# Kernel tuning notes

Measured on AMD Instinct MI355X. Metric: run time of the kernel, lower is better.

The kernel has to match this reference:

```python
import jax, jax.numpy as jnp
import numpy as np

TEMPERATURE = 0.07
N, D, NUM_CLASSES = 8192, 1024, 128


def setup_inputs() -> dict:
    key = jax.random.key(0)
    k1, k2 = jax.random.split(key)
    embeddings = jax.random.normal(k1, (N, D), dtype=jnp.float32)
    labels = jax.random.randint(k2, (N,), 0, NUM_CLASSES, dtype=jnp.int64)
    return {"embeddings": embeddings, "labels": labels}


def reference(embeddings, labels):
    # L2-normalize rows (eps matches F.normalize default clamp of 1e-12 on the norm)
    norm = jnp.maximum(jnp.linalg.norm(embeddings, axis=-1, keepdims=True), 1e-12)
    emb = embeddings / norm
    # [N, N] similarity scaled by temperature
    sim = jnp.matmul(emb, emb.T) / TEMPERATURE
    # positive mask: same label, diagonal zeroed
    pos_mask = (labels[:, None] == labels[None, :]).astype(sim.dtype)
    pos_mask = pos_mask * (1.0 - jnp.eye(sim.shape[0], dtype=sim.dtype))
    exp_sim = jnp.exp(sim)
    sum_exp = exp_sim.sum(axis=1)              # [N]
    pos_sum = (exp_sim * pos_mask).sum(axis=1)  # [N]
    loss = -jnp.log(pos_sum / sum_exp)
    return loss.mean()
```

## Files before the change

kernel.cpp:

```cpp
#include <hip/hip_runtime.h>
#include <hip/hip_bf16.h>
#include <math.h>

#define N 8192
#define D 1024
#define BM 256
#define BK 64
#define NQUART 64
#define NFULL 512
#define NBLK (NQUART + NFULL)
#define ITERS 8

typedef __bf16 bf16_t;
typedef bf16_t bf16x4 __attribute__((ext_vector_type(4)));
typedef bf16_t bf16x8 __attribute__((ext_vector_type(8)));
typedef float f32x4 __attribute__((ext_vector_type(4)));

__global__ __launch_bounds__(256) void norm_cast(const float* __restrict__ in,
                                                 bf16_t* __restrict__ out,
                                                 float* __restrict__ sumExp,
                                                 float* __restrict__ posSum) {
    const int wave = threadIdx.x >> 6, lane = threadIdx.x & 63;
    const int row  = blockIdx.x * 4 + wave;
    const float4* src = (const float4*)(in + (size_t)row * D);
    float4 v[4];
    float ss = 0.f;
    #pragma unroll
    for (int i = 0; i < 4; ++i) {
        v[i] = src[lane + 64 * i];
        ss += v[i].x * v[i].x + v[i].y * v[i].y + v[i].z * v[i].z + v[i].w * v[i].w;
    }
    #pragma unroll
    for (int off = 32; off >= 1; off >>= 1) ss += __shfl_xor(ss, off, 64);
    const float scale = 1.0f / fmaxf(sqrtf(ss), 1e-12f);
    bf16x4* dst = (bf16x4*)(out + (size_t)row * D);
    #pragma unroll
    for (int i = 0; i < 4; ++i) {
        bf16x4 o;
        o[0] = (bf16_t)(v[i].x * scale);
        o[1] = (bf16_t)(v[i].y * scale);
        o[2] = (bf16_t)(v[i].z * scale);
        o[3] = (bf16_t)(v[i].w * scale);
        dst[lane + 64 * i] = o;
    }
    if (lane == 0) { sumExp[row] = 0.f; posSum[row] = 0.f; }
}

__global__ __launch_bounds__(512, 2) void gemm_fused(const bf16_t* __restrict__ E,
                                                     const int* __restrict__ labels,
                                                     float* __restrict__ sumExp,
                                                     float* __restrict__ posSum) {
    __shared__ bf16_t As[2][2][128 * 64];
    __shared__ bf16_t Bs[2][2][128 * 64];

    const int tid  = threadIdx.x;
    const int wave = tid >> 6;
    const int lane = tid & 63;
    const int lr   = lane & 15;
    const int q    = lane >> 4;
    const float invT = 1.0f / 0.07f;

    const int su0 = ((0 + q) ^ (lane & 7)) * 16;
    const int su1 = ((4 + q) ^ (lane & 7)) * 16;

    #define PHASE_MID() do {                                                             \
        __builtin_amdgcn_s_barrier();                                                    \
        asm volatile("s_waitcnt lgkmcnt(0)");                                            \
        __builtin_amdgcn_sched_barrier(0);                                               \
        __builtin_amdgcn_s_setprio(1);                                                   \
    } while (0)
    #define PHASE_END() do {                                                             \
        __builtin_amdgcn_s_setprio(0);                                                   \
        __builtin_amdgcn_s_barrier();                                                    \
    } while (0)

    if (blockIdx.x < NQUART) {
        const int qb = ((int)blockIdx.x & 7) * 8 + ((int)blockIdx.x >> 3);
        const int p  = qb >> 2, qd = qb & 3;
        const int rowStart = 31 * BM + (qd >> 1) * 128;
        const int colStart = p * BM + (qd & 1) * 128;
        const int wm2 = wave >> 2;
        const int wn2 = wave & 3;

        f32x4 acc[4][2];
        #pragma unroll
        for (int m = 0; m < 4; ++m) { acc[m][0] = {0,0,0,0}; acc[m][1] = {0,0,0,0}; }

        const int r0  = tid >> 3;
        const int lu0 = (tid & 7) ^ (r0 & 7);
        const char* gA = (const char*)(E + (size_t)rowStart * D) + (size_t)r0 * (D * 2) + lu0 * 16;
        const char* gB = (const char*)(E + (size_t)colStart * D) + (size_t)r0 * (D * 2) + lu0 * 16;

        #define QSTAGE(buf, kb) do {                                                     \
            const char* ga_ = gA + (kb);                                                 \
            const char* gb_ = gB + (kb);                                                 \
            char* la_ = (char*)&As[buf][0][0] + wave * 1024;                             \
            char* lb_ = (char*)&Bs[buf][0][0] + wave * 1024;                             \
            __builtin_amdgcn_global_load_lds((const __attribute__((address_space(1))) void*)ga_, \
                (__attribute__((address_space(3))) void*)la_, 16, 0, 0);                 \
            __builtin_amdgcn_global_load_lds(                                            \
                (const __attribute__((address_space(1))) void*)(ga_ + 64 * 2048),        \
                (__attribute__((address_space(3))) void*)(la_ + 8192), 16, 0, 0);        \
            __builtin_amdgcn_global_load_lds((const __attribute__((address_space(1))) void*)gb_, \
                (__attribute__((address_space(3))) void*)lb_, 16, 0, 0);                 \
            __builtin_amdgcn_global_load_lds(                                            \
                (const __attribute__((address_space(1))) void*)(gb_ + 64 * 2048),        \
                (__attribute__((address_space(3))) void*)(lb_ + 8192), 16, 0, 0);        \
        } while (0)

        bf16x8 qa[4], qbf[2];
        #define QLD(SU, BUF) do {                                                        \
            const char* aB_ = (const char*)&As[BUF][0][0] + (wm2 * 64 + lr) * 128 + (SU);\
            const char* bB_ = (const char*)&Bs[BUF][0][0] + (wn2 * 32 + lr) * 128 + (SU);\
            _Pragma("unroll")                                                            \
            for (int m_ = 0; m_ < 4; ++m_)                                               \
                qa[m_] = *(const bf16x8*)(aB_ + m_ * 2048);                              \
            qbf[0] = *(const bf16x8*)(bB_);                                              \
            qbf[1] = *(const bf16x8*)(bB_ + 2048);                                       \
        } while (0)
        #define QMFMA() do {                                                             \
            _Pragma("unroll")                                                            \
            for (int m_ = 0; m_ < 4; ++m_) {                                             \
                _Pragma("unroll")                                                        \
                for (int n_ = 0; n_ < 2; ++n_)                                           \
                    acc[m_][n_] = __builtin_amdgcn_mfma_f32_16x16x32_bf16(               \
                        qa[m_], qbf[n_], acc[m_][n_], 0, 0, 0);                          \
            }                                                                            \
        } while (0)

        QSTAGE(0, 0);
        asm volatile("s_waitcnt vmcnt(0)" ::: "memory");
        __builtin_amdgcn_sched_barrier(0);
        __builtin_amdgcn_s_barrier();

        #pragma unroll 1
        for (int it = 0; it < 16; ++it) {
            const int buf = it & 1;
            QLD(su0, buf);
            if (it < 15) QSTAGE(buf ^ 1, (it + 1) * 128);
            PHASE_MID();
            QMFMA();
            PHASE_END();
            QLD(su1, buf);
            asm volatile("s_waitcnt vmcnt(0)" ::: "memory");
            __builtin_amdgcn_sched_barrier(0);
            PHASE_MID();
            QMFMA();
            PHASE_END();
        }

        int lc[2];
        lc[0] = labels[colStart + wn2 * 32 + lr];
        lc[1] = labels[colStart + wn2 * 32 + 16 + lr];
        float colAll[2] = {0.f, 0.f}, colPos[2] = {0.f, 0.f};
        #pragma unroll
        for (int m = 0; m < 4; ++m) {
            #pragma unroll
            for (int e = 0; e < 4; ++e) {
                const int gi = rowStart + wm2 * 64 + m * 16 + q * 4 + e;
                const int li = labels[gi];
                float s_all = 0.f, s_pos = 0.f;
                #pragma unroll
                for (int n = 0; n < 2; ++n) {
                    const float v = __expf(acc[m][n][e] * invT);
                    const bool same = (lc[n] == li);
                    s_all += v;
                    if (same) s_pos += v;
                    colAll[n] += v;
                    if (same) colPos[n] += v;
                }
                #pragma unroll
                for (int off = 1; off < 16; off <<= 1) {
                    s_all += __shfl_xor(s_all, off, 64);
                    s_pos += __shfl_xor(s_pos, off, 64);
                }
                if (lr == 0) {
                    atomicAdd(&sumExp[gi], s_all);
                    atomicAdd(&posSum[gi], s_pos);
                }
            }
        }
        #pragma unroll
        for (int n = 0; n < 2; ++n) {
            float a = colAll[n], pp = colPos[n];
            a += __shfl_xor(a, 16, 64);  a += __shfl_xor(a, 32, 64);
            pp += __shfl_xor(pp, 16, 64); pp += __shfl_xor(pp, 32, 64);
            if (q == 0) {
                const int gj = colStart + wn2 * 32 + n * 16 + lr;
                atomicAdd(&sumExp[gj], a);
                atomicAdd(&posSum[gj], pp);
            }
        }
        return;
    }

    const int f0 = (int)blockIdx.x - NQUART;
    const int f  = (f0 & 7) * (NFULL / 8) + (f0 >> 3);
    const int b  = (f < 496) ? f : f + 16;

    int ti = (int)((sqrtf(8.0f * (float)b + 1.0f) - 1.0f) * 0.5f);
    while ((ti + 1) * (ti + 2) / 2 <= b) ++ti;
    while (ti * (ti + 1) / 2 > b) --ti;
    const int tj = b - ti * (ti + 1) / 2;
    const bool isDiag = (ti == tj);

    const int wm   = wave >> 2;
    const int wn   = wave & 3;
    const int rowStart = ti * BM;
    const int colStart = tj * BM;

    f32x4 acc[8][4];
    #pragma unroll
    for (int m = 0; m < 8; ++m)
        #pragma unroll
        for (int n = 0; n < 4; ++n) acc[m][n] = {0.f, 0.f, 0.f, 0.f};

    const int r0  = tid >> 3;
    const int lu0 = (tid & 7) ^ (r0 & 7);
    const char* gA = (const char*)(E + (size_t)rowStart * D) + (size_t)r0 * (D * 2) + lu0 * 16;
    const char* gB = (const char*)(E + (size_t)colStart * D) + (size_t)r0 * (D * 2) + lu0 * 16;

    #define STAGE_A(buf, h, kb) do {                                                     \
        const char* g0_ = gA + (size_t)(h) * (128 * 2048) + (kb);                        \
        char* l0_ = (char*)&As[buf][h][0] + wave * 1024;                                 \
        __builtin_amdgcn_global_load_lds((const __attribute__((address_space(1))) void*)g0_, \
            (__attribute__((address_space(3))) void*)l0_, 16, 0, 0);                     \
        __builtin_amdgcn_global_load_lds(                                                \
            (const __attribute__((address_space(1))) void*)(g0_ + 64 * 2048),            \
            (__attribute__((address_space(3))) void*)(l0_ + 8192), 16, 0, 0);            \
    } while (0)
    #define STAGE_B(buf, h, kb) do {                                                     \
        const char* g0_ = gB + (size_t)(h) * (128 * 2048) + (kb);                        \
        char* l0_ = (char*)&Bs[buf][h][0] + wave * 1024;                                 \
        __builtin_amdgcn_global_load_lds((const __attribute__((address_space(1))) void*)g0_, \
            (__attribute__((address_space(3))) void*)l0_, 16, 0, 0);                     \
        __builtin_amdgcn_global_load_lds(                                                \
            (const __attribute__((address_space(1))) void*)(g0_ + 64 * 2048),            \
            (__attribute__((address_space(3))) void*)(l0_ + 8192), 16, 0, 0);            \
    } while (0)

    const char* rA0 = (const char*)&As[0][wm][0] + lr * 128;
    const char* rA1 = (const char*)&As[1][wm][0] + lr * 128;
    const char* rB0 = (const char*)&Bs[0][wn >> 1][0] + (wn & 1) * 8192 + lr * 128;
    const char* rB1 = (const char*)&Bs[1][wn >> 1][0] + (wn & 1) * 8192 + lr * 128;

    #define LD_A4(DST, RBASE, MOFFB, SU) do {                                            \
        _Pragma("unroll")                                                                \
        for (int m_ = 0; m_ < 4; ++m_)                                                   \
            DST[m_] = *(const bf16x8*)((RBASE) + (MOFFB) + m_ * 2048 + (SU));            \
    } while (0)
    #define LD_B4(DST, RBASE, SU) do {                                                   \
        _Pragma("unroll")                                                                \
        for (int n_ = 0; n_ < 4; ++n_)                                                   \
            DST[n_] = *(const bf16x8*)((RBASE) + n_ * 2048 + (SU));                      \
    } while (0)
    #define MFMA_QUAD(AF, BF, MO) do {                                                   \
        _Pragma("unroll")                                                                \
        for (int m_ = 0; m_ < 4; ++m_) {                                                 \
            _Pragma("unroll")                                                            \
            for (int n_ = 0; n_ < 4; ++n_)                                               \
                acc[(MO) + m_][n_] = __builtin_amdgcn_mfma_f32_16x16x32_bf16(            \
                    AF[m_], BF[n_], acc[(MO) + m_][n_], 0, 0, 0);                        \
        }                                                                                \
    } while (0)

    bf16x8 a0[4], a1[4], bq0[4], bq1[4];

    STAGE_B(0, 0, 0);  STAGE_B(0, 1, 0);
    STAGE_A(0, 0, 0);  STAGE_A(0, 1, 0);
    STAGE_B(1, 0, 128); STAGE_B(1, 1, 128);
    asm volatile("s_waitcnt vmcnt(4)" ::: "memory");
    __builtin_amdgcn_sched_barrier(0);
    __builtin_amdgcn_s_barrier();

    #pragma unroll 1
    for (int it = 0; it < ITERS; ++it) {
        const bool lastIt = (it == ITERS - 1);
        const int kb1 = (2 * it + 1) * 128;
        const int kb2 = (2 * it + 2) * 128;
        const int kb3 = (2 * it + 3) * 128;

        LD_A4(a0, rA0, 0, su0);
        LD_B4(bq0, rB0, su0);
        STAGE_A(1, 0, kb1);
        PHASE_MID();
        MFMA_QUAD(a0, bq0, 0);
        PHASE_END();

        LD_A4(a1, rA0, 0, su1);
        LD_B4(bq1, rB0, su1);
        STAGE_A(1, 1, kb1);
        PHASE_MID();
        MFMA_QUAD(a1, bq1, 0);
        PHASE_END();

        LD_A4(a0, rA0, 8192, su0);
        if (!lastIt) STAGE_B(0, 0, kb2);
        PHASE_MID();
        MFMA_QUAD(a0, bq0, 4);
        PHASE_END();

        LD_A4(a1, rA0, 8192, su1);
        if (!lastIt) {
            STAGE_B(0, 1, kb2);
            asm volatile("s_waitcnt vmcnt(4)" ::: "memory");
        } else {
            asm volatile("s_waitcnt vmcnt(0)" ::: "memory");
        }
        __builtin_amdgcn_sched_barrier(0);
        PHASE_MID();
        MFMA_QUAD(a1, bq1, 4);
        PHASE_END();

        LD_A4(a0, rA1, 0, su0);
        LD_B4(bq0, rB1, su0);
        if (!lastIt) STAGE_A(0, 0, kb2);
        PHASE_MID();
        MFMA_QUAD(a0, bq0, 0);
        PHASE_END();

        LD_A4(a1, rA1, 0, su1);
        LD_B4(bq1, rB1, su1);
        if (!lastIt) STAGE_A(0, 1, kb2);
        PHASE_MID();
        MFMA_QUAD(a1, bq1, 0);
        PHASE_END();

        LD_A4(a0, rA1, 8192, su0);
        if (!lastIt) STAGE_B(1, 0, kb3);
        PHASE_MID();
        MFMA_QUAD(a0, bq0, 4);
        PHASE_END();

        LD_A4(a1, rA1, 8192, su1);
        if (!lastIt) {
            STAGE_B(1, 1, kb3);
            asm volatile("s_waitcnt vmcnt(4)" ::: "memory");
            __builtin_amdgcn_sched_barrier(0);
        }
        PHASE_MID();
        MFMA_QUAD(a1, bq1, 4);
        PHASE_END();
    }

    int lc[4];
    #pragma unroll
    for (int n = 0; n < 4; ++n)
        lc[n] = labels[colStart + wn * 64 + n * 16 + lr];

    float colAll[4] = {0.f, 0.f, 0.f, 0.f};
    float colPos[4] = {0.f, 0.f, 0.f, 0.f};
    #pragma unroll
    for (int m = 0; m < 8; ++m) {
        #pragma unroll
        for (int e = 0; e < 4; ++e) {
            const int rloc = wm * 128 + m * 16 + q * 4 + e;
            const int gi   = rowStart + rloc;
            const int li   = labels[gi];
            float s_all = 0.f, s_pos = 0.f;
            #pragma unroll
            for (int n = 0; n < 4; ++n) {
                const int cloc = wn * 64 + n * 16 + lr;
                const int gj   = colStart + cloc;
                const float v  = __expf(acc[m][n][e] * invT);
                const bool same = (lc[n] == li);
                s_all += v;
                if (same && gi != gj) s_pos += v;
                if (!isDiag) {
                    colAll[n] += v;
                    if (same) colPos[n] += v;
                }
            }
            #pragma unroll
            for (int off = 1; off < 16; off <<= 1) {
                s_all += __shfl_xor(s_all, off, 64);
                s_pos += __shfl_xor(s_pos, off, 64);
            }
            if (lr == 0) {
                atomicAdd(&sumExp[gi], s_all);
                atomicAdd(&posSum[gi], s_pos);
            }
        }
    }
    if (!isDiag) {
        #pragma unroll
        for (int n = 0; n < 4; ++n) {
            float a = colAll[n], p = colPos[n];
            a += __shfl_xor(a, 16, 64);  a += __shfl_xor(a, 32, 64);
            p += __shfl_xor(p, 16, 64);  p += __shfl_xor(p, 32, 64);
            if (q == 0) {
                const int gj = colStart + wn * 64 + n * 16 + lr;
                atomicAdd(&sumExp[gj], a);
                atomicAdd(&posSum[gj], p);
            }
        }
    }
}

__global__ __launch_bounds__(1024) void finalize(const float* __restrict__ sumExp,
                                                 const float* __restrict__ posSum,
                                                 float* __restrict__ out) {
    const int tid = threadIdx.x;
    float s = 0.f;
    #pragma unroll
    for (int i = tid; i < N; i += 1024)
        s += __logf(sumExp[i] / posSum[i]);
    #pragma unroll
    for (int off = 32; off >= 1; off >>= 1) s += __shfl_xor(s, off, 64);
    __shared__ float red[16];
    if ((tid & 63) == 0) red[tid >> 6] = s;
    __syncthreads();
    if (tid == 0) {
        float t = 0.f;
        #pragma unroll
        for (int i = 0; i < 16; ++i) t += red[i];
        out[0] = t / (float)N;
    }
}

extern "C" void kernel_launch(void* const* d_in, const int* in_sizes, int n_in,
                              void* d_out, int out_size, void* d_ws, size_t ws_size,
                              hipStream_t stream) {
    const float* emb    = (const float*)d_in[0];
    const int*   labels = (const int*)d_in[1];
    float* out = (float*)d_out;

    float*  sumExp = (float*)d_ws;
    float*  posSum = sumExp + N;
    bf16_t* EN     = (bf16_t*)((char*)d_ws + (size_t)2 * N * sizeof(float));

    norm_cast<<<N / 4, 256, 0, stream>>>(emb, EN, sumExp, posSum);

    gemm_fused<<<NBLK, 512, 0, stream>>>(EN, labels, sumExp, posSum);

    finalize<<<1, 1024, 0, stream>>>(sumExp, posSum, out);
}
```

Baseline: 206.7 us.

## Triple-buffer quarter-tile loads and fold finalize into GEMM via last-block reduction

The quarter-tile path moves from a double-buffered to a three-slot LDS ring with two stages in flight, waiting on vmcnt(4) instead of draining all loads each iteration. The separate finalize kernel is removed. Instead, each GEMM block bumps a global counter after a threadfence, and the last block to finish reduces the log ratios and writes the mean. This saves one kernel launch and hides more load latency, at the cost of a serialized tail reduction inside the last block and an extra atomic per block.

```diff
diff --git a/kernel.cpp b/kernel.cpp
--- a/kernel.cpp
+++ b/kernel.cpp
@@ -19,9 +19,11 @@
 __global__ __launch_bounds__(256) void norm_cast(const float* __restrict__ in,
                                                  bf16_t* __restrict__ out,
                                                  float* __restrict__ sumExp,
-                                                 float* __restrict__ posSum) {
+                                                 float* __restrict__ posSum,
+                                                 int* __restrict__ cnt) {
     const int wave = threadIdx.x >> 6, lane = threadIdx.x & 63;
     const int row  = blockIdx.x * 4 + wave;
+    if (blockIdx.x == 0 && threadIdx.x == 0) *cnt = 0;
     const float4* src = (const float4*)(in + (size_t)row * D);
     float4 v[4];
     float ss = 0.f;
@@ -49,7 +51,9 @@
 __global__ __launch_bounds__(512, 2) void gemm_fused(const bf16_t* __restrict__ E,
                                                      const int* __restrict__ labels,
                                                      float* __restrict__ sumExp,
-                                                     float* __restrict__ posSum) {
+                                                     float* __restrict__ posSum,
+                                                     float* __restrict__ out,
+                                                     int* __restrict__ cnt) {
     __shared__ bf16_t As[2][2][128 * 64];
     __shared__ bf16_t Bs[2][2][128 * 64];
 
@@ -81,6 +85,8 @@
         const int colStart = p * BM + (qd & 1) * 128;
         const int wm2 = wave >> 2;
         const int wn2 = wave & 3;
+        char* Aflat = (char*)&As[0][0][0];
+        char* Bflat = (char*)&Bs[0][0][0];
 
         f32x4 acc[4][2];
         #pragma unroll
@@ -91,11 +97,11 @@
         const char* gA = (const char*)(E + (size_t)rowStart * D) + (size_t)r0 * (D * 2) + lu0 * 16;
         const char* gB = (const char*)(E + (size_t)colStart * D) + (size_t)r0 * (D * 2) + lu0 * 16;
 
-        #define QSTAGE(buf, kb) do {                                                     \
+        #define QSTAGE(slot, kb) do {                                                    \
             const char* ga_ = gA + (kb);                                                 \
             const char* gb_ = gB + (kb);                                                 \
-            char* la_ = (char*)&As[buf][0][0] + wave * 1024;                             \
-            char* lb_ = (char*)&Bs[buf][0][0] + wave * 1024;                             \
+            char* la_ = Aflat + (slot) * 16384 + wave * 1024;                            \
+            char* lb_ = Bflat + (slot) * 16384 + wave * 1024;                            \
             __builtin_amdgcn_global_load_lds((const __attribute__((address_space(1))) void*)ga_, \
                 (__attribute__((address_space(3))) void*)la_, 16, 0, 0);                 \
             __builtin_amdgcn_global_load_lds(                                            \
@@ -109,9 +115,9 @@
         } while (0)
 
         bf16x8 qa[4], qbf[2];
-        #define QLD(SU, BUF) do {                                                        \
-            const char* aB_ = (const char*)&As[BUF][0][0] + (wm2 * 64 + lr) * 128 + (SU);\
-            const char* bB_ = (const char*)&Bs[BUF][0][0] + (wn2 * 32 + lr) * 128 + (SU);\
+        #define QLD(SU, slot) do {                                                       \
+            const char* aB_ = Aflat + (slot) * 16384 + (wm2 * 64 + lr) * 128 + (SU);     \
+            const char* bB_ = Bflat + (slot) * 16384 + (wn2 * 32 + lr) * 128 + (SU);     \
             _Pragma("unroll")                                                            \
             for (int m_ = 0; m_ < 4; ++m_)                                               \
                 qa[m_] = *(const bf16x8*)(aB_ + m_ * 2048);                              \
@@ -129,20 +135,22 @@
         } while (0)
 
         QSTAGE(0, 0);
-        asm volatile("s_waitcnt vmcnt(0)" ::: "memory");
+        QSTAGE(1, 128);
+        asm volatile("s_waitcnt vmcnt(4)" ::: "memory");
         __builtin_amdgcn_sched_barrier(0);
         __builtin_amdgcn_s_barrier();
 
         #pragma unroll 1
         for (int it = 0; it < 16; ++it) {
-            const int buf = it & 1;
-            QLD(su0, buf);
-            if (it < 15) QSTAGE(buf ^ 1, (it + 1) * 128);
+            const int slot = it % 3;
+            QLD(su0, slot);
+            if (it < 14) QSTAGE((it + 2) % 3, (it + 2) * 128);
             PHASE_MID();
             QMFMA();
             PHASE_END();
-            QLD(su1, buf);
-            asm volatile("s_waitcnt vmcnt(0)" ::: "memory");
+            QLD(su1, slot);
+            if (it < 14) asm volatile("s_waitcnt vmcnt(4)" ::: "memory");
+            else         asm volatile("s_waitcnt vmcnt(0)" ::: "memory");
             __builtin_amdgcn_sched_barrier(0);
             PHASE_MID();
             QMFMA();
@@ -191,9 +199,7 @@
                 atomicAdd(&posSum[gj], pp);
             }
         }
-        return;
-    }
-
+    } else {
     const int f0 = (int)blockIdx.x - NQUART;
     const int f  = (f0 & 7) * (NFULL / 8) + (f0 >> 3);
     const int b  = (f < 496) ? f : f + 16;
@@ -395,26 +401,34 @@
             }
         }
     }
-}
-
-__global__ __launch_bounds__(1024) void finalize(const float* __restrict__ sumExp,
-                                                 const float* __restrict__ posSum,
-                                                 float* __restrict__ out) {
-    const int tid = threadIdx.x;
-    float s = 0.f;
-    #pragma unroll
-    for (int i = tid; i < N; i += 1024)
-        s += __logf(sumExp[i] / posSum[i]);
-    #pragma unroll
-    for (int off = 32; off >= 1; off >>= 1) s += __shfl_xor(s, off, 64);
-    __shared__ float red[16];
-    if ((tid & 63) == 0) red[tid >> 6] = s;
+    }
+
+    __threadfence();
     __syncthreads();
-    if (tid == 0) {
-        float t = 0.f;
-        #pragma unroll
-        for (int i = 0; i < 16; ++i) t += red[i];
-        out[0] = t / (float)N;
+    int* lastFlag = (int*)&As[0][0][0];
+    float* redf   = (float*)&As[0][0][64];
+    if (tid == 0) *lastFlag = (atomicAdd(cnt, 1) == NBLK - 1) ? 1 : 0;
+    __syncthreads();
+    if (*lastFlag) {
+        float s = 0.f;
+        #pragma unroll
+        for (int i = tid; i < N; i += 512) {
+            const float se = __hip_atomic_load(&sumExp[i], __ATOMIC_RELAXED,
+                                               __HIP_MEMORY_SCOPE_AGENT);
+            const float ps = __hip_atomic_load(&posSum[i], __ATOMIC_RELAXED,
+                                               __HIP_MEMORY_SCOPE_AGENT);
+            s += __logf(se / ps);
+        }
+        #pragma unroll
+        for (int off = 32; off >= 1; off >>= 1) s += __shfl_xor(s, off, 64);
+        if (lane == 0) redf[wave] = s;
+        __syncthreads();
+        if (tid == 0) {
+            float t = 0.f;
+            #pragma unroll
+            for (int i = 0; i < 8; ++i) t += redf[i];
+            out[0] = t / (float)N;
+        }
     }
 }
 
@@ -427,11 +441,10 @@
 
     float*  sumExp = (float*)d_ws;
     float*  posSum = sumExp + N;
-    bf16_t* EN     = (bf16_t*)((char*)d_ws + (size_t)2 * N * sizeof(float));
-
-    norm_cast<<<N / 4, 256, 0, stream>>>(emb, EN, sumExp, posSum);
-
-    gemm_fused<<<NBLK, 512, 0, stream>>>(EN, labels, sumExp, posSum);
-
-    finalize<<<1, 1024, 0, stream>>>(sumExp, posSum, out);
+    int*    cnt    = (int*)((char*)d_ws + (size_t)2 * N * sizeof(float));
+    bf16_t* EN     = (bf16_t*)((char*)d_ws + (size_t)2 * N * sizeof(float) + 16);
+
+    norm_cast<<<N / 4, 256, 0, stream>>>(emb, EN, sumExp, posSum, cnt);
+
+    gemm_fused<<<NBLK, 512, 0, stream>>>(EN, labels, sumExp, posSum, out, cnt);
 }
```

Measured after the change: 309.2 us. 1.5x slower.

## Move quarter tiles to end of grid and stage 128-wide K slabs

Applied to the files above, without the earlier changes.

The 64 small quarter-tile blocks now run after the 512 full blocks instead of before them, and their K loop stages 128-element slabs (8 iterations instead of 16). Each stage is consumed with four unrolled K-chunks and a single barrier per slab, replacing the per-half priority/barrier phases. The aim is fewer barriers and less loop overhead in the tail blocks, and better tail filling by the smaller tiles. The catch is larger LDS slabs per stage, and the quarter blocks no longer use the XCD-interleaved index remap.

```diff
diff --git a/kernel.cpp b/kernel.cpp
--- a/kernel.cpp
+++ b/kernel.cpp
@@ -74,79 +74,72 @@
         __builtin_amdgcn_s_barrier();                                                    \
     } while (0)
 
-    if (blockIdx.x < NQUART) {
-        const int qb = ((int)blockIdx.x & 7) * 8 + ((int)blockIdx.x >> 3);
+    if (blockIdx.x >= NFULL) {
+        const int qb = (int)blockIdx.x - NFULL;
         const int p  = qb >> 2, qd = qb & 3;
         const int rowStart = 31 * BM + (qd >> 1) * 128;
         const int colStart = p * BM + (qd & 1) * 128;
         const int wm2 = wave >> 2;
         const int wn2 = wave & 3;
+        char* Aflat = (char*)&As[0][0][0];
+        char* Bflat = (char*)&Bs[0][0][0];
 
         f32x4 acc[4][2];
         #pragma unroll
         for (int m = 0; m < 4; ++m) { acc[m][0] = {0,0,0,0}; acc[m][1] = {0,0,0,0}; }
 
-        const int r0  = tid >> 3;
-        const int lu0 = (tid & 7) ^ (r0 & 7);
-        const char* gA = (const char*)(E + (size_t)rowStart * D) + (size_t)r0 * (D * 2) + lu0 * 16;
-        const char* gB = (const char*)(E + (size_t)colStart * D) + (size_t)r0 * (D * 2) + lu0 * 16;
-
-        #define QSTAGE(buf, kb) do {                                                     \
-            const char* ga_ = gA + (kb);                                                 \
-            const char* gb_ = gB + (kb);                                                 \
-            char* la_ = (char*)&As[buf][0][0] + wave * 1024;                             \
-            char* lb_ = (char*)&Bs[buf][0][0] + wave * 1024;                             \
-            __builtin_amdgcn_global_load_lds((const __attribute__((address_space(1))) void*)ga_, \
-                (__attribute__((address_space(3))) void*)la_, 16, 0, 0);                 \
-            __builtin_amdgcn_global_load_lds(                                            \
-                (const __attribute__((address_space(1))) void*)(ga_ + 64 * 2048),        \
-                (__attribute__((address_space(3))) void*)(la_ + 8192), 16, 0, 0);        \
-            __builtin_amdgcn_global_load_lds((const __attribute__((address_space(1))) void*)gb_, \
-                (__attribute__((address_space(3))) void*)lb_, 16, 0, 0);                 \
-            __builtin_amdgcn_global_load_lds(                                            \
-                (const __attribute__((address_space(1))) void*)(gb_ + 64 * 2048),        \
-                (__attribute__((address_space(3))) void*)(lb_ + 8192), 16, 0, 0);        \
-        } while (0)
-
-        bf16x8 qa[4], qbf[2];
-        #define QLD(SU, BUF) do {                                                        \
-            const char* aB_ = (const char*)&As[BUF][0][0] + (wm2 * 64 + lr) * 128 + (SU);\
-            const char* bB_ = (const char*)&Bs[BUF][0][0] + (wn2 * 32 + lr) * 128 + (SU);\
+        const int r0 = tid >> 4;
+        const int lu = (tid & 15) ^ (r0 & 7);
+        const char* gA = (const char*)(E + (size_t)rowStart * D) + (size_t)r0 * 2048 + lu * 16;
+        const char* gB = (const char*)(E + (size_t)colStart * D) + (size_t)r0 * 2048 + lu * 16;
+
+        #define Q128STAGE(bi, t) do {                                                    \
+            const char* ga_ = gA + (t) * 256;                                            \
+            const char* gb_ = gB + (t) * 256;                                            \
+            char* la_ = Aflat + (bi) * 32768 + wave * 1024;                              \
+            char* lb_ = Bflat + (bi) * 32768 + wave * 1024;                              \
             _Pragma("unroll")                                                            \
-            for (int m_ = 0; m_ < 4; ++m_)                                               \
-                qa[m_] = *(const bf16x8*)(aB_ + m_ * 2048);                              \
-            qbf[0] = *(const bf16x8*)(bB_);                                              \
-            qbf[1] = *(const bf16x8*)(bB_ + 2048);                                       \
-        } while (0)
-        #define QMFMA() do {                                                             \
-            _Pragma("unroll")                                                            \
-            for (int m_ = 0; m_ < 4; ++m_) {                                             \
-                _Pragma("unroll")                                                        \
-                for (int n_ = 0; n_ < 2; ++n_)                                           \
-                    acc[m_][n_] = __builtin_amdgcn_mfma_f32_16x16x32_bf16(               \
-                        qa[m_], qbf[n_], acc[m_][n_], 0, 0, 0);                          \
+            for (int g_ = 0; g_ < 4; ++g_) {                                             \
+                __builtin_amdgcn_global_load_lds(                                        \
+                    (const __attribute__((address_space(1))) void*)(ga_ + g_ * 32 * 2048), \
+                    (__attribute__((address_space(3))) void*)(la_ + g_ * 8192), 16, 0, 0); \
+                __builtin_amdgcn_global_load_lds(                                        \
+                    (const __attribute__((address_space(1))) void*)(gb_ + g_ * 32 * 2048), \
+                    (__attribute__((address_space(3))) void*)(lb_ + g_ * 8192), 16, 0, 0); \
             }                                                                            \
         } while (0)
 
-        QSTAGE(0, 0);
+        Q128STAGE(0, 0);
         asm volatile("s_waitcnt vmcnt(0)" ::: "memory");
         __builtin_amdgcn_sched_barrier(0);
         __builtin_amdgcn_s_barrier();
 
         #pragma unroll 1
-        for (int it = 0; it < 16; ++it) {
-            const int buf = it & 1;
-            QLD(su0, buf);
-            if (it < 15) QSTAGE(buf ^ 1, (it + 1) * 128);
-            PHASE_MID();
-            QMFMA();
-            PHASE_END();
-            QLD(su1, buf);
+        for (int s = 0; s < 8; ++s) {
+            const int buf = s & 1;
+            if (s < 7) Q128STAGE(buf ^ 1, s + 1);
+            const char* aB = Aflat + buf * 32768 + (wm2 * 64 + lr) * 256;
+            const char* bB = Bflat + buf * 32768 + (wn2 * 32 + lr) * 256;
+            #pragma unroll
+            for (int kc = 0; kc < 4; ++kc) {
+                const int su_ = ((kc * 4 + q) ^ (lane & 7)) * 16;
+                bf16x8 qa[4], qbv[2];
+                #pragma unroll
+                for (int m_ = 0; m_ < 4; ++m_)
+                    qa[m_] = *(const bf16x8*)(aB + m_ * 4096 + su_);
+                qbv[0] = *(const bf16x8*)(bB + su_);
+                qbv[1] = *(const bf16x8*)(bB + 4096 + su_);
+                #pragma unroll
+                for (int m_ = 0; m_ < 4; ++m_) {
+                    #pragma unroll
+                    for (int n_ = 0; n_ < 2; ++n_)
+                        acc[m_][n_] = __builtin_amdgcn_mfma_f32_16x16x32_bf16(
+                            qa[m_], qbv[n_], acc[m_][n_], 0, 0, 0);
+                }
+            }
             asm volatile("s_waitcnt vmcnt(0)" ::: "memory");
             __builtin_amdgcn_sched_barrier(0);
-            PHASE_MID();
-            QMFMA();
-            PHASE_END();
+            __builtin_amdgcn_s_barrier();
         }
 
         int lc[2];
@@ -194,7 +187,7 @@
         return;
     }
 
-    const int f0 = (int)blockIdx.x - NQUART;
+    const int f0 = (int)blockIdx.x;
     const int f  = (f0 & 7) * (NFULL / 8) + (f0 >> 3);
     const int b  = (f < 496) ? f : f + 16;
 
```

New measurement: 208.2 us. No clear change (+0.7%).
